# Kernel tuning notes

Hardware: AMD Instinct MI355X
Metric: run time of the kernel (lower is better)

The kernel has to match this reference:

```python
import jax, jax.numpy as jnp
import numpy as np

B = 16384
H = 1024

def setup_inputs() -> dict:
    key = jax.random.key(0)
    k1, k2, k3, k4, k5 = jax.random.split(key, 5)
    inp = jax.random.normal(k1, (B, 3 * H), dtype=jnp.float32)
    previous_state = jax.random.normal(k2, (B, H), dtype=jnp.float32)
    mask = jax.random.uniform(k3, (B,), dtype=jnp.float32)
    # params: th_normal scale 0.08
    Wur = 0.08 * jax.random.normal(k4, (H, 2 * H), dtype=jnp.float32)
    U = 0.08 * jax.random.normal(k5, (H, H), dtype=jnp.float32)
    return {"inp": inp, "previous_state": previous_state, "mask": mask, "Wur": Wur, "U": U}

def reference(inp, previous_state, mask, Wur, U):
    h = U.shape[0]
    state_inp = inp[:, :h]            # [B, H]
    gate_inp = inp[:, h:]             # [B, 2H]
    gates = jax.nn.sigmoid(previous_state @ Wur + gate_inp)  # [B, 2H]
    update = gates[:, :h]
    reset = gates[:, h:]
    p = (state_inp * reset) @ U       # [B, H]
    next_state = jnp.tanh(p + state_inp)
    # NOTE: faithful to source (additive combine, not convex blend)
    next_state_f = next_state + update + (previous_state + (1.0 - update))
    m = mask[:, None]
    return m * next_state_f + (1.0 - m) * previous_state
```

## Files before the change

kernel.cpp:

```cpp
#include <hip/hip_runtime.h>
#include <cstdint>
#include <cstddef>

#define DI __device__ __forceinline__

typedef __attribute__((ext_vector_type(8))) short short8;
typedef __attribute__((ext_vector_type(4))) float floatx4;

static constexpr int BATCH = 16384;
static constexpr int H = 1024;
static constexpr int NT = H / 64;
static constexpr int HALF = 128 * 64;

DI unsigned short f32_to_bf16_bits(float x) {
  union { float f; unsigned int u; } c; c.f = x;
  unsigned int r = c.u + 0x7fffu + ((c.u >> 16) & 1u);
  return (unsigned short)(r >> 16);
}

__global__ __launch_bounds__(256) void transpose_cast2_kernel(const float* __restrict__ Wur,
                                                              const float* __restrict__ U,
                                                              unsigned short* __restrict__ WrT,
                                                              unsigned short* __restrict__ UT) {
  __shared__ float tile[32][33];
  const float* in;
  unsigned short* out;
  int src_stride, src_col0;
  if (blockIdx.z == 0) {
    in = Wur; out = WrT; src_stride = 2 * H; src_col0 = H;
  } else {
    in = U; out = UT; src_stride = H; src_col0 = 0;
  }
  const int bx = blockIdx.x * 32;
  const int by = blockIdx.y * 32;
  const int tx = threadIdx.x;
  const int ty = threadIdx.y;
#pragma unroll
  for (int i = 0; i < 32; i += 8)
    tile[ty + i][tx] = in[(size_t)(bx + ty + i) * src_stride + src_col0 + by + tx];
  __syncthreads();
#pragma unroll
  for (int i = 0; i < 32; i += 8)
    out[(size_t)(by + ty + i) * H + bx + tx] = f32_to_bf16_bits(tile[tx][ty + i]);
}

__global__ __launch_bounds__(256, 2) void gemm_k1(const float* __restrict__ prevf,
                                                  const unsigned short* __restrict__ Bt,
                                                  const float* __restrict__ inp,
                                                  unsigned short* __restrict__ Xout) {
  __shared__ __align__(16) unsigned short ldsA[2][128 * 64];
  __shared__ __align__(16) unsigned short ldsB[2][128 * 64];

  const int tid = threadIdx.x;
  const int lane = tid & 63;
  const int wave = tid >> 6;
  const int wm = wave >> 1;
  const int wn = wave & 1;
  const int q = lane >> 4;
  const int l16 = lane & 15;

  const int sid = blockIdx.y * gridDim.x + blockIdx.x;
  const int lid = (sid & 7) * 128 + (sid >> 3);
  const int bx = lid & 7;
  const int by = lid >> 3;
  const int blockM = by * 128;
  const int blockN = bx * 128;

  int aRow[4], aKlog[4], bSrc[4], bDst[4];
#pragma unroll
  for (int j = 0; j < 4; ++j) {
    const int c = j * 256 + tid;
    const int r = c >> 3;
    aRow[j] = r;
    aKlog[j] = ((c & 7) ^ (r & 7)) * 8;
    bSrc[j] = r * H + aKlog[j];
    bDst[j] = (j * 256 + (wave << 6)) * 8;
  }

  auto issueA = [&](int kt, float4* st) {
#pragma unroll
    for (int j = 0; j < 4; ++j) {
      const float* s = prevf + (size_t)(blockM + aRow[j]) * H + kt + aKlog[j];
      st[2 * j] = *reinterpret_cast<const float4*>(s);
      st[2 * j + 1] = *reinterpret_cast<const float4*>(s + 4);
    }
  };
  auto issueB = [&](int kt, int buf) {
#pragma unroll
    for (int j = 0; j < 4; ++j) {
      __builtin_amdgcn_global_load_lds(
          (const __attribute__((address_space(1))) unsigned int*)(Bt + (size_t)blockN * H + kt + bSrc[j]),
          (__attribute__((address_space(3))) unsigned int*)(&ldsB[buf][bDst[j]]), 16, 0, 0);
    }
  };
  auto writeA = [&](const float4* st, int buf) {
#pragma unroll
    for (int j = 0; j < 4; ++j) {
      const int c = j * 256 + tid;
      short8 o;
      o[0] = (short)f32_to_bf16_bits(st[2 * j].x);
      o[1] = (short)f32_to_bf16_bits(st[2 * j].y);
      o[2] = (short)f32_to_bf16_bits(st[2 * j].z);
      o[3] = (short)f32_to_bf16_bits(st[2 * j].w);
      o[4] = (short)f32_to_bf16_bits(st[2 * j + 1].x);
      o[5] = (short)f32_to_bf16_bits(st[2 * j + 1].y);
      o[6] = (short)f32_to_bf16_bits(st[2 * j + 1].z);
      o[7] = (short)f32_to_bf16_bits(st[2 * j + 1].w);
      *reinterpret_cast<short8*>(&ldsA[buf][c * 8]) = o;
    }
  };

  floatx4 acc[4][4] = {};
  float4 st[8];

  issueA(0, st);
  issueB(0, 0);
  writeA(st, 0);
  __syncthreads();

  for (int t = 0; t < NT; ++t) {
    const int cur = t & 1;
    const int kn = ((t + 1) & (NT - 1)) * 64;
    issueA(kn, st);
    issueB(kn, cur ^ 1);

#pragma unroll
    for (int ks = 0; ks < 2; ++ks) {
      short8 af[4], bfr[4];
#pragma unroll
      for (int i = 0; i < 4; ++i) {
        const int r = wm * 64 + i * 16 + l16;
        const int ch = ks * 4 + q;
        af[i] = *(const short8*)&ldsA[cur][(r * 8 + (ch ^ (r & 7))) * 8];
      }
#pragma unroll
      for (int j = 0; j < 4; ++j) {
        const int r = wn * 64 + j * 16 + l16;
        const int ch = ks * 4 + q;
        bfr[j] = *(const short8*)&ldsB[cur][(r * 8 + (ch ^ (r & 7))) * 8];
      }
#pragma unroll
      for (int i = 0; i < 4; ++i)
#pragma unroll
        for (int j = 0; j < 4; ++j)
          acc[i][j] = __builtin_amdgcn_mfma_f32_16x16x32_bf16(af[i], bfr[j], acc[i][j], 0, 0, 0);
    }

    writeA(st, cur ^ 1);
    __syncthreads();
  }

#pragma unroll
  for (int i = 0; i < 4; ++i) {
    const int gr0 = blockM + wm * 64 + i * 16 + q * 4;
#pragma unroll
    for (int j = 0; j < 4; ++j) {
      const int gcol = blockN + wn * 64 + j * 16 + l16;
#pragma unroll
      for (int rg = 0; rg < 4; ++rg) {
        const int gr = gr0 + rg;
        const float z = acc[i][j][rg] + inp[(size_t)gr * (3 * H) + 2 * H + gcol];
        const float rst = 1.0f / (1.0f + __expf(-z));
        const float x = inp[(size_t)gr * (3 * H) + gcol] * rst;
        Xout[(size_t)gr * H + gcol] = f32_to_bf16_bits(x);
      }
    }
  }
}

DI void ld8(short8* fr, const unsigned short* base, int wofs, int l16, int q) {
  const int x7 = l16 & 7;
#pragma unroll
  for (int f = 0; f < 4; ++f) {
    const int lr = 32 * f + wofs + l16;
#pragma unroll
    for (int ks = 0; ks < 2; ++ks)
      fr[f * 2 + ks] = *(const short8*)&base[lr * 64 + (((ks * 4 + q) ^ x7) * 8)];
  }
}
DI void ld4(short8* fr, const unsigned short* base, int wofs, int l16, int q) {
  const int x7 = l16 & 7;
#pragma unroll
  for (int jj = 0; jj < 2; ++jj) {
    const int lc = 64 * jj + wofs + l16;
#pragma unroll
    for (int ks = 0; ks < 2; ++ks)
      fr[jj * 2 + ks] = *(const short8*)&base[lc * 64 + (((ks * 4 + q) ^ x7) * 8)];
  }
}

template <int IO, int JO>
DI void mma16(floatx4 (&acc)[8][4], const short8* af, const short8* bf) {
#pragma unroll
  for (int ks = 0; ks < 2; ++ks)
#pragma unroll
    for (int f = 0; f < 4; ++f)
#pragma unroll
      for (int jj = 0; jj < 2; ++jj)
        acc[IO + f][JO + jj] = __builtin_amdgcn_mfma_f32_16x16x32_bf16(
            af[f * 2 + ks], bf[jj * 2 + ks], acc[IO + f][JO + jj], 0, 0, 0);
}

__global__ __launch_bounds__(512, 2) void gemm_k2(const unsigned short* __restrict__ A,
                                                  const unsigned short* __restrict__ Bt,
                                                  const float* __restrict__ inp,
                                                  const float* __restrict__ prev,
                                                  const float* __restrict__ mask,
                                                  float* __restrict__ Out) {
  __shared__ __align__(16) unsigned short ldsA[2 * 2 * HALF];
  __shared__ __align__(16) unsigned short ldsB[2 * 2 * HALF];

  const int tid = threadIdx.x;
  const int lane = tid & 63;
  const int w = tid >> 6;
  const int wm16 = (w >> 2) * 16;
  const int wn16 = (w & 3) * 16;
  const int q = lane >> 4;
  const int l16 = lane & 15;

  const int sid = blockIdx.y * gridDim.x + blockIdx.x;
  const int lid = (sid & 7) * 32 + (sid >> 3);
  const int blockN = (lid & 3) * 256;
  const int blockM = (lid >> 2) * 256;

  int srcoff[2], dstch[2];
#pragma unroll
  for (int n = 0; n < 2; ++n) {
    const int c = n * 512 + tid;
    const int r = c >> 3;
    const int gc = (c & 7) ^ (r & 7);
    srcoff[n] = r * H + gc * 8;
    dstch[n] = n * 512 + w * 64;
  }

  const unsigned short* Ab = A + (size_t)blockM * H;
  const unsigned short* Bb = Bt + (size_t)blockN * H;

  auto stage = [&](const unsigned short* gsrc, unsigned short* ldst) {
#pragma unroll
    for (int n = 0; n < 2; ++n) {
      __builtin_amdgcn_global_load_lds(
          (const __attribute__((address_space(1))) unsigned int*)(gsrc + srcoff[n]),
          (__attribute__((address_space(3))) unsigned int*)(ldst + dstch[n] * 8), 16, 0, 0);
    }
  };

  floatx4 acc[8][4] = {};
  short8 af[8], bf0[4], bf1[4];

  stage(Ab, ldsA);
  stage(Bb, ldsB);
  stage(Bb + 128 * H, ldsB + HALF);
  stage(Ab + 128 * H, ldsA + HALF);
  asm volatile("s_waitcnt vmcnt(4)" ::: "memory");
  __builtin_amdgcn_s_barrier();

  for (int t = 0; t < NT; ++t) {
    const int cur = t & 1;
    const int kn = ((t + 1) & (NT - 1)) * 64;
    const unsigned short* lAc = ldsA + cur * 2 * HALF;
    const unsigned short* lBc = ldsB + cur * 2 * HALF;
    unsigned short* lAn = ldsA + (cur ^ 1) * 2 * HALF;
    unsigned short* lBn = ldsB + (cur ^ 1) * 2 * HALF;

    ld8(af, lAc, wm16, l16, q);
    ld4(bf0, lBc, wn16, l16, q);
    stage(Ab + kn, lAn);
    __builtin_amdgcn_s_barrier();
    __builtin_amdgcn_s_setprio(1);
    mma16<0, 0>(acc, af, bf0);
    __builtin_amdgcn_s_setprio(0);
    asm volatile("s_waitcnt vmcnt(4)" ::: "memory");
    __builtin_amdgcn_s_barrier();

    ld4(bf1, lBc + HALF, wn16, l16, q);
    stage(Bb + kn, lBn);
    __builtin_amdgcn_s_barrier();
    __builtin_amdgcn_s_setprio(1);
    mma16<0, 2>(acc, af, bf1);
    __builtin_amdgcn_s_setprio(0);
    asm volatile("s_waitcnt vmcnt(4)" ::: "memory");
    __builtin_amdgcn_s_barrier();

    ld8(af, lAc + HALF, wm16, l16, q);
    stage(Bb + 128 * H + kn, lBn + HALF);
    __builtin_amdgcn_s_barrier();
    __builtin_amdgcn_s_setprio(1);
    mma16<4, 2>(acc, af, bf1);
    __builtin_amdgcn_s_setprio(0);
    __builtin_amdgcn_s_barrier();

    stage(Ab + 128 * H + kn, lAn + HALF);
    __builtin_amdgcn_s_barrier();
    __builtin_amdgcn_s_setprio(1);
    mma16<4, 0>(acc, af, bf0);
    __builtin_amdgcn_s_setprio(0);
    asm volatile("s_waitcnt vmcnt(4)" ::: "memory");
    __builtin_amdgcn_s_barrier();
  }

#pragma unroll
  for (int i = 0; i < 8; ++i) {
    const int gr0 = blockM + 128 * (i >> 2) + 32 * (i & 3) + wm16 + q * 4;
#pragma unroll
    for (int j = 0; j < 4; ++j) {
      const int gcol = blockN + 128 * (j >> 1) + 64 * (j & 1) + wn16 + l16;
#pragma unroll
      for (int rg = 0; rg < 4; ++rg) {
        const int gr = gr0 + rg;
        const float s = inp[(size_t)gr * (3 * H) + gcol];
        const float a = acc[i][j][rg] + s;
        const float ns = 1.0f - 2.0f / (__expf(2.0f * a) + 1.0f);
        const float m = mask[gr];
        Out[(size_t)gr * H + gcol] = m * (ns + 1.0f) + prev[(size_t)gr * H + gcol];
      }
    }
  }
}

extern "C" void kernel_launch(void* const* d_in, const int* in_sizes, int n_in,
                              void* d_out, int out_size, void* d_ws, size_t ws_size,
                              hipStream_t stream) {
  const float* inp = (const float*)d_in[0];
  const float* prev = (const float*)d_in[1];
  const float* mask = (const float*)d_in[2];
  const float* Wur = (const float*)d_in[3];
  const float* U = (const float*)d_in[4];
  float* out = (float*)d_out;

  char* ws = (char*)d_ws;
  unsigned short* Xb = (unsigned short*)ws;
  unsigned short* WrT = (unsigned short*)(ws + (size_t)BATCH * H * 2);
  unsigned short* UT = WrT + (size_t)H * H;

  transpose_cast2_kernel<<<dim3(H / 32, H / 32, 2), dim3(32, 8), 0, stream>>>(Wur, U, WrT, UT);

  gemm_k1<<<dim3(H / 128, BATCH / 128), 256, 0, stream>>>(prev, WrT, inp, Xb);

  gemm_k2<<<dim3(H / 256, BATCH / 256), 512, 0, stream>>>(Xb, UT, inp, prev, mask, out);
}
```

Measured before the change: 459.1 us.

## Load fp32 A tile directly to LDS, single-buffer, raise occupancy to 3

The first GEMM kernel now streams the fp32 previous_state tile into LDS with global_load_lds instead of going through registers, and converts to bf16 when reading fragments from LDS. Double buffering is dropped in favour of a single buffer with a full vmcnt wait and barrier each K-step, and launch bounds allow three blocks per CU. The aim is to cut register pressure and VGPR staging so occupancy can hide latency instead of explicit prefetch. The trade-offs are more LDS traffic per fragment (fp32 reads), repeated conversion work in the inner loop, and no overlap of loads with compute within a block.

```diff
diff --git a/kernel.cpp b/kernel.cpp
--- a/kernel.cpp
+++ b/kernel.cpp
@@ -44,12 +44,12 @@
     out[(size_t)(by + ty + i) * H + bx + tx] = f32_to_bf16_bits(tile[tx][ty + i]);
 }
 
-__global__ __launch_bounds__(256, 2) void gemm_k1(const float* __restrict__ prevf,
+__global__ __launch_bounds__(256, 3) void gemm_k1(const float* __restrict__ prevf,
                                                   const unsigned short* __restrict__ Bt,
                                                   const float* __restrict__ inp,
                                                   unsigned short* __restrict__ Xout) {
-  __shared__ __align__(16) unsigned short ldsA[2][128 * 64];
-  __shared__ __align__(16) unsigned short ldsB[2][128 * 64];
+  __shared__ __align__(16) float ldsAf[128 * 64];
+  __shared__ __align__(16) unsigned short ldsB[128 * 64];
 
   const int tid = threadIdx.x;
   const int lane = tid & 63;
@@ -66,78 +66,66 @@
   const int blockM = by * 128;
   const int blockN = bx * 128;
 
-  int aRow[4], aKlog[4], bSrc[4], bDst[4];
+  int aSrc[8], aDst[8], bSrc[4], bDst[4];
+#pragma unroll
+  for (int j = 0; j < 8; ++j) {
+    const int c = j * 256 + tid;
+    const int r = c >> 4;
+    aSrc[j] = r * H + ((c & 15) ^ (r & 15)) * 4;
+    aDst[j] = (j * 256 + (wave << 6)) * 4;
+  }
 #pragma unroll
   for (int j = 0; j < 4; ++j) {
     const int c = j * 256 + tid;
     const int r = c >> 3;
-    aRow[j] = r;
-    aKlog[j] = ((c & 7) ^ (r & 7)) * 8;
-    bSrc[j] = r * H + aKlog[j];
+    bSrc[j] = r * H + ((c & 7) ^ (r & 7)) * 8;
     bDst[j] = (j * 256 + (wave << 6)) * 8;
   }
 
-  auto issueA = [&](int kt, float4* st) {
-#pragma unroll
-    for (int j = 0; j < 4; ++j) {
-      const float* s = prevf + (size_t)(blockM + aRow[j]) * H + kt + aKlog[j];
-      st[2 * j] = *reinterpret_cast<const float4*>(s);
-      st[2 * j + 1] = *reinterpret_cast<const float4*>(s + 4);
-    }
-  };
-  auto issueB = [&](int kt, int buf) {
+  floatx4 acc[4][4] = {};
+
+  for (int kt = 0; kt < H; kt += 64) {
+#pragma unroll
+    for (int j = 0; j < 8; ++j) {
+      __builtin_amdgcn_global_load_lds(
+          (const __attribute__((address_space(1))) unsigned int*)(prevf + (size_t)blockM * H + kt + aSrc[j]),
+          (__attribute__((address_space(3))) unsigned int*)(&ldsAf[aDst[j]]), 16, 0, 0);
+    }
 #pragma unroll
     for (int j = 0; j < 4; ++j) {
       __builtin_amdgcn_global_load_lds(
           (const __attribute__((address_space(1))) unsigned int*)(Bt + (size_t)blockN * H + kt + bSrc[j]),
-          (__attribute__((address_space(3))) unsigned int*)(&ldsB[buf][bDst[j]]), 16, 0, 0);
-    }
-  };
-  auto writeA = [&](const float4* st, int buf) {
-#pragma unroll
-    for (int j = 0; j < 4; ++j) {
-      const int c = j * 256 + tid;
-      short8 o;
-      o[0] = (short)f32_to_bf16_bits(st[2 * j].x);
-      o[1] = (short)f32_to_bf16_bits(st[2 * j].y);
-      o[2] = (short)f32_to_bf16_bits(st[2 * j].z);
-      o[3] = (short)f32_to_bf16_bits(st[2 * j].w);
-      o[4] = (short)f32_to_bf16_bits(st[2 * j + 1].x);
-      o[5] = (short)f32_to_bf16_bits(st[2 * j + 1].y);
-      o[6] = (short)f32_to_bf16_bits(st[2 * j + 1].z);
-      o[7] = (short)f32_to_bf16_bits(st[2 * j + 1].w);
-      *reinterpret_cast<short8*>(&ldsA[buf][c * 8]) = o;
-    }
-  };
-
-  floatx4 acc[4][4] = {};
-  float4 st[8];
-
-  issueA(0, st);
-  issueB(0, 0);
-  writeA(st, 0);
-  __syncthreads();
-
-  for (int t = 0; t < NT; ++t) {
-    const int cur = t & 1;
-    const int kn = ((t + 1) & (NT - 1)) * 64;
-    issueA(kn, st);
-    issueB(kn, cur ^ 1);
+          (__attribute__((address_space(3))) unsigned int*)(&ldsB[bDst[j]]), 16, 0, 0);
+    }
+    asm volatile("s_waitcnt vmcnt(0)" ::: "memory");
+    __syncthreads();
 
 #pragma unroll
     for (int ks = 0; ks < 2; ++ks) {
       short8 af[4], bfr[4];
 #pragma unroll
       for (int i = 0; i < 4; ++i) {
-        const int r = wm * 64 + i * 16 + l16;
-        const int ch = ks * 4 + q;
-        af[i] = *(const short8*)&ldsA[cur][(r * 8 + (ch ^ (r & 7))) * 8];
+        const int lr = wm * 64 + i * 16 + l16;
+        const int lc0 = (ks * 4 + q) * 2;
+        const int x = lr & 15;
+        const float4 lo = *(const float4*)&ldsAf[lr * 64 + ((lc0 ^ x) * 4)];
+        const float4 hi = *(const float4*)&ldsAf[lr * 64 + (((lc0 + 1) ^ x) * 4)];
+        short8 a;
+        a[0] = (short)f32_to_bf16_bits(lo.x);
+        a[1] = (short)f32_to_bf16_bits(lo.y);
+        a[2] = (short)f32_to_bf16_bits(lo.z);
+        a[3] = (short)f32_to_bf16_bits(lo.w);
+        a[4] = (short)f32_to_bf16_bits(hi.x);
+        a[5] = (short)f32_to_bf16_bits(hi.y);
+        a[6] = (short)f32_to_bf16_bits(hi.z);
+        a[7] = (short)f32_to_bf16_bits(hi.w);
+        af[i] = a;
       }
 #pragma unroll
       for (int j = 0; j < 4; ++j) {
         const int r = wn * 64 + j * 16 + l16;
         const int ch = ks * 4 + q;
-        bfr[j] = *(const short8*)&ldsB[cur][(r * 8 + (ch ^ (r & 7))) * 8];
+        bfr[j] = *(const short8*)&ldsB[(r * 8 + (ch ^ (r & 7))) * 8];
       }
 #pragma unroll
       for (int i = 0; i < 4; ++i)
@@ -145,8 +133,6 @@
         for (int j = 0; j < 4; ++j)
           acc[i][j] = __builtin_amdgcn_mfma_f32_16x16x32_bf16(af[i], bfr[j], acc[i][j], 0, 0, 0);
     }
-
-    writeA(st, cur ^ 1);
     __syncthreads();
   }
 
```

Result: faster. 442.5 us (-3.6%).
